# Performance work log

Measured on AMD Instinct MI355X. Metric: run time of the kernel, lower is better.

## Reference

```python
import jax, jax.numpy as jnp
import numpy as np

N_NEAR = 16
BN_EPS = 1e-5


def fps(xyz, n_center):
    # farthest point sampling, deterministic start at index 0. xyz: [B,N,C]
    B, N, _ = xyz.shape
    dist0 = jnp.full((B, N), jnp.inf, dtype=xyz.dtype)
    far0 = jnp.zeros((B,), dtype=jnp.int32)

    def step(carry, _):
        dist, far = carry
        centroid = jnp.take_along_axis(xyz, far[:, None, None], axis=1)  # [B,1,C]
        d = jnp.sum((xyz - centroid) ** 2, axis=-1)                       # [B,N]
        dist = jnp.minimum(dist, d)
        nxt = jnp.argmax(dist, axis=-1).astype(jnp.int32)
        return (dist, nxt), far

    _, idxs = jax.lax.scan(step, (dist0, far0), None, length=n_center)
    return jnp.transpose(idxs)  # [B, n_center]


def knn(xyz, k):
    # k nearest neighbors (self included), xyz: [B,N,C] -> idx [B,N,k]
    sq = jnp.sum(xyz * xyz, axis=-1)
    d = sq[:, :, None] - 2.0 * jnp.einsum('bnc,bmc->bnm', xyz, xyz) + sq[:, None, :]
    _, idx = jax.lax.top_k(-d, k)
    return idx


def gather_points(x, idx):
    # x: [B,N,...], idx: [B,*dims] int -> [B,*dims,...]
    return jax.vmap(lambda xb, ib: xb[ib])(x, idx)


def conv_bn_relu(x, W, b, g, be):
    # x: [B,C,K,S]; 1x1 Conv2d + BatchNorm2d (training/batch stats) + ReLU
    y = jnp.einsum('oc,bcks->boks', W, x) + b[None, :, None, None]
    mean = jnp.mean(y, axis=(0, 2, 3), keepdims=True)
    var = jnp.mean((y - mean) ** 2, axis=(0, 2, 3), keepdims=True)  # biased var, as torch BN
    y = (y - mean) * jax.lax.rsqrt(var + BN_EPS)
    y = y * g[None, :, None, None] + be[None, :, None, None]
    return jax.nn.relu(y)


def setup_inputs() -> dict:
    key = jax.random.key(0)
    ks = jax.random.split(key, 8)
    B, N, EMB = 16, 2048, 64
    mlp = [64, 128, 256]
    in_ch = 2 + EMB
    inp = {
        'xy': jax.random.normal(ks[0], (B, 2, N), dtype=jnp.float32),
        'fea': jax.random.normal(ks[1], (B, EMB, N), dtype=jnp.float32),
    }
    last = in_ch
    for i, out in enumerate(mlp):
        inp[f'W{i+1}'] = 0.1 * jax.random.normal(ks[2 + i], (out, last), dtype=jnp.float32)
        inp[f'b{i+1}'] = jnp.zeros((out,), dtype=jnp.float32)
        inp[f'g{i+1}'] = jnp.ones((out,), dtype=jnp.float32)
        inp[f'be{i+1}'] = jnp.zeros((out,), dtype=jnp.float32)
        last = out
    return inp


def reference(xy, fea, W1, b1, g1, be1, W2, b2, g2, be2, W3, b3, g3, be3):
    B, _, N = xy.shape
    n_center = N // 2 + 1
    xyz = jnp.transpose(xy, (0, 2, 1))   # [B,N,2]
    f = jnp.transpose(fea, (0, 2, 1))    # [B,N,emb]

    fps_idx = fps(xyz, n_center)                      # [B,S]
    new_xyz = gather_points(xyz, fps_idx)             # [B,S,2]
    knn_idx = knn(xyz, N_NEAR)                        # [B,N,k]
    knn_of_fps = gather_points(knn_idx, fps_idx)      # [B,S,k]
    grouped_xyz = gather_points(xyz, knn_of_fps)      # [B,S,k,2]
    grouped_norm = grouped_xyz - new_xyz[:, :, None, :]
    grouped_f = gather_points(f, knn_of_fps)          # [B,S,k,emb]
    new_fea = jnp.concatenate([grouped_norm, grouped_f], axis=-1)  # [B,S,k,C]

    x = jnp.transpose(new_fea, (0, 3, 2, 1))          # [B,C,k,S]
    for (W, b, g, be) in ((W1, b1, g1, be1), (W2, b2, g2, be2), (W3, b3, g3, be3)):
        x = conv_bn_relu(x, W, b, g, be)
    out = jnp.max(x, axis=2)                          # [B,C_out,S]
    return jnp.transpose(new_xyz, (0, 2, 1)), out
```

## Files before the change

### kernel.cpp

```cpp
#include <hip/hip_runtime.h>
#include <math.h>

#define B_   16
#define N_   2048
#define S_   1025
#define K_   16
#define EMB_ 64
#define NF_  (B_ * S_ * K_)
#define NCH_ (NF_ / 64)

typedef float v2f __attribute__((ext_vector_type(2)));
typedef short bf16x8 __attribute__((ext_vector_type(8)));
typedef float f32x4 __attribute__((ext_vector_type(4)));

__device__ __forceinline__ unsigned short f2bf(float f) {
  unsigned u = __float_as_uint(f);
  u += 0x7fffu + ((u >> 16) & 1u);
  return (unsigned short)(u >> 16);
}

__global__ __launch_bounds__(256) __attribute__((amdgpu_waves_per_eu(1, 1)))
void fps_pk_kernel(const float* __restrict__ xy, const float* __restrict__ fea,
                   const float* __restrict__ W1,
                   int* __restrict__ fps_idx, float* __restrict__ new_xyz,
                   float* __restrict__ out0, float* __restrict__ P) {
  __shared__ float smem[8192];
  if (blockIdx.x < 16) {
    const int b = blockIdx.x;
    float2* lxy = reinterpret_cast<float2*>(smem);
    const int lane = threadIdx.x;
    const float* xb = xy + (size_t)b * 2 * N_;
    v2f pxp[16], pyp[16];
    float dist[32];
    if (lane < 64) {
      const float2* xb2 = (const float2*)xb;
      const float2* yb2 = (const float2*)(xb + N_);
#pragma unroll
      for (int q = 0; q < 16; ++q) {
        float2 x01 = xb2[lane * 16 + q];
        float2 y01 = yb2[lane * 16 + q];
        int p = lane * 32 + 2 * q;
        lxy[p] = make_float2(x01.x, y01.x);
        lxy[p + 1] = make_float2(x01.y, y01.y);
        pxp[q][0] = x01.x; pxp[q][1] = x01.y;
        pyp[q][0] = y01.x; pyp[q][1] = y01.y;
        dist[2 * q] = __builtin_inff();
        dist[2 * q + 1] = __builtin_inff();
      }
#pragma unroll
      for (int q = 0; q < 16; ++q) {
        asm volatile("" : "+v"(pxp[q]), "+v"(pyp[q]));
      }
    }
    __syncthreads();
    if (lane < 64) {
      int cur = 0;
      for (int t = 0; t < S_; ++t) {
        float2 c = lxy[cur];
        if (lane == 0) {
          fps_idx[b * S_ + t] = cur;
          new_xyz[(b * S_ + t) * 2 + 0] = c.x;
          new_xyz[(b * S_ + t) * 2 + 1] = c.y;
          out0[b * 2 * S_ + t] = c.x;
          out0[b * 2 * S_ + S_ + t] = c.y;
        }
        const float ncx = -c.x, ncy = -c.y;
        v2f ncx2; ncx2[0] = ncx; ncx2[1] = ncx;
        v2f ncy2; ncy2[0] = ncy; ncy2[1] = ncy;
        float lmax0 = -__builtin_inff(), lmax1 = -__builtin_inff();
#pragma unroll
        for (int q = 0; q < 16; ++q) {
          v2f dx, dy, sx, sy, dd;
          asm("v_pk_add_f32 %0, %1, %2" : "=v"(dx) : "v"(pxp[q]), "v"(ncx2));
          asm("v_pk_add_f32 %0, %1, %2" : "=v"(dy) : "v"(pyp[q]), "v"(ncy2));
          asm("v_pk_mul_f32 %0, %1, %1" : "=v"(sx) : "v"(dx));
          asm("v_pk_mul_f32 %0, %1, %1" : "=v"(sy) : "v"(dy));
          asm("v_pk_add_f32 %0, %1, %2" : "=v"(dd) : "v"(sx), "v"(sy));
          float nd0 = fminf(dist[2 * q], dd[0]);
          float nd1 = fminf(dist[2 * q + 1], dd[1]);
          dist[2 * q] = nd0;
          dist[2 * q + 1] = nd1;
          lmax0 = fmaxf(lmax0, nd0);
          lmax1 = fmaxf(lmax1, nd1);
        }
        const float lmax = fmaxf(lmax0, lmax1);
        int xr = __float_as_int(lmax);
#define DPP_MAX_STEP(CTRL)                                                        \
        {                                                                         \
          int tmp_ = __builtin_amdgcn_update_dpp(xr, xr, (CTRL), 0xF, 0xF, false);\
          xr = __float_as_int(fmaxf(__int_as_float(xr), __int_as_float(tmp_)));   \
        }
        DPP_MAX_STEP(0x111)
        DPP_MAX_STEP(0x112)
        DPP_MAX_STEP(0x114)
        DPP_MAX_STEP(0x118)
        DPP_MAX_STEP(0x142)
        DPP_MAX_STEP(0x143)
#undef DPP_MAX_STEP
        const float g = __int_as_float(__builtin_amdgcn_readlane(xr, 63));
        int lf = 0;
#pragma unroll
        for (int j = 31; j >= 0; --j)
          if (dist[j] == g) lf = j;
        unsigned long long mask = __ballot(lmax == g);
        int first = __ffsll(mask) - 1;
        cur = __builtin_amdgcn_readlane(lane * 32 + lf, first);
      }
    }
  } else {
    const int bid = blockIdx.x - 16;
    const int t = threadIdx.x;
    const int b = bid >> 5;
    const int pt0 = (bid & 31) << 6;
    float* W1L = smem;
    float* feaL = smem + 4096;
#pragma unroll
    for (int p = 0; p < 16; ++p) {
      int idx = t + 256 * p;
      int c = idx >> 6, e = idx & 63;
      W1L[e * 64 + c] = W1[c * 66 + 2 + e];
      int r = (t >> 6) + 4 * p, cc = t & 63;
      feaL[r * 64 + cc] = fea[((size_t)b * 64 + r) * N_ + pt0 + cc];
    }
    __syncthreads();
    const int tpt = t & 15, tcq = t >> 4;
    float acc[4][4];
#pragma unroll
    for (int i = 0; i < 4; ++i)
#pragma unroll
      for (int j = 0; j < 4; ++j) acc[i][j] = 0.f;
    for (int e = 0; e < 64; ++e) {
      float4 a4 = *reinterpret_cast<const float4*>(&W1L[e * 64 + tcq * 4]);
      float4 b4 = *reinterpret_cast<const float4*>(&feaL[e * 64 + tpt * 4]);
      const float av[4] = {a4.x, a4.y, a4.z, a4.w};
      const float bvv[4] = {b4.x, b4.y, b4.z, b4.w};
#pragma unroll
      for (int i = 0; i < 4; ++i)
#pragma unroll
        for (int j = 0; j < 4; ++j) acc[i][j] = fmaf(av[i], bvv[j], acc[i][j]);
    }
#pragma unroll
    for (int j = 0; j < 4; ++j) {
      int pt = tpt * 4 + j;
      float4 v = {acc[0][j], acc[1][j], acc[2][j], acc[3][j]};
      *reinterpret_cast<float4*>(&P[((size_t)(b * N_ + pt0 + pt)) * 64 + tcq * 4]) = v;
    }
  }
}

__global__ void wconv_kernel(const float* __restrict__ W2, const float* __restrict__ W3,
                             unsigned short* __restrict__ W2b, unsigned short* __restrict__ W3b) {
  int i = blockIdx.x * 256 + threadIdx.x;
  if (i < 128 * 64) W2b[i] = f2bf(W2[i]);
  if (i < 256 * 128) W3b[i] = f2bf(W3[i]);
}

__global__ __launch_bounds__(256) void knn_kernel(const float* __restrict__ xy,
                                                  const int* __restrict__ fps_idx,
                                                  int* __restrict__ knn_sel) {
  const int b = blockIdx.y;
  __shared__ float2 lxy[N_];
  __shared__ double lsq[N_];
  const float* xb = xy + (size_t)b * 2 * N_;
  for (int p = threadIdx.x; p < N_; p += 256) {
    float x = xb[p], y = xb[N_ + p];
    lxy[p] = make_float2(x, y);
    lsq[p] = (double)x * (double)x + (double)y * (double)y;
  }
  __syncthreads();
  const int t = threadIdx.x;
  const int s = blockIdx.x * 16 + (t >> 4);
  if (s >= S_) return;
  const int oct = t & 15;
  const int p0 = fps_idx[b * S_ + s];
  float2 q = lxy[p0];
  const double xn = (double)q.x, yn = (double)q.y;
  const double sqn = lsq[p0];
  double d16[16];
  int i16[16];
#pragma unroll
  for (int j = 0; j < 16; ++j) { d16[j] = __builtin_inf(); i16[j] = 0x7fffffff; }
  const int mlo = oct * 128;
  for (int m0 = mlo; m0 < mlo + 128; m0 += 4) {
    double dd[4];
#pragma unroll
    for (int u = 0; u < 4; ++u) {
      float2 p = lxy[m0 + u];
      double dot = (double)p.x * xn + (double)p.y * yn;
      dd[u] = (sqn - 2.0 * dot) + lsq[m0 + u];
    }
#pragma unroll
    for (int u = 0; u < 4; ++u) {
      if (dd[u] < d16[15]) {
        double d = dd[u];
        int mi = m0 + u;
#pragma unroll
        for (int j = 15; j >= 1; --j) {
          bool shift = d < d16[j - 1];
          bool ins = d < d16[j];
          d16[j] = shift ? d16[j - 1] : (ins ? d : d16[j]);
          i16[j] = shift ? i16[j - 1] : (ins ? mi : i16[j]);
        }
        if (d < d16[0]) { d16[0] = d; i16[0] = mi; }
      }
    }
  }
#pragma unroll
  for (int w = 1; w <= 8; w <<= 1) {
    double nd[16]; int ni[16];
#pragma unroll
    for (int i = 0; i < 16; ++i) {
      double rd = __shfl_xor(d16[15 - i], w, 64);
      int ri = __shfl_xor(i16[15 - i], w, 64);
      bool takeR = (rd < d16[i]) || (rd == d16[i] && ri < i16[i]);
      nd[i] = takeR ? rd : d16[i];
      ni[i] = takeR ? ri : i16[i];
    }
#pragma unroll
    for (int i = 0; i < 16; ++i) { d16[i] = nd[i]; i16[i] = ni[i]; }
    if (w < 8) {
#pragma unroll
      for (int dstg = 8; dstg >= 1; dstg >>= 1) {
#pragma unroll
        for (int i = 0; i < 16; ++i) {
          if ((i & dstg) == 0) {
            int a = i, c = i + dstg;
            bool sw = (d16[a] > d16[c]) || (d16[a] == d16[c] && i16[a] > i16[c]);
            double tlo = sw ? d16[c] : d16[a];
            double thi = sw ? d16[a] : d16[c];
            int ulo = sw ? i16[c] : i16[a];
            int uhi = sw ? i16[a] : i16[c];
            d16[a] = tlo; d16[c] = thi; i16[a] = ulo; i16[c] = uhi;
          }
        }
      }
    }
  }
  if (oct == 0) {
    int* dst = knn_sel + ((size_t)b * S_ + s) * K_;
#pragma unroll
    for (int j = 0; j < 16; ++j) dst[j] = i16[j];
  }
}

__global__ __launch_bounds__(256) void yk1_kernel(const float* __restrict__ xy,
                                                  const int* __restrict__ knn_sel,
                                                  const float* __restrict__ new_xyz,
                                                  const float* __restrict__ P,
                                                  const float* __restrict__ W1,
                                                  const float* __restrict__ b1,
                                                  float* __restrict__ Y1) {
  __shared__ float w0s[64], w1s[64], bbs[64];
  const int t = threadIdx.x;
  if (t < 64) { w0s[t] = W1[t * 66 + 0]; w1s[t] = W1[t * 66 + 1]; bbs[t] = b1[t]; }
  __syncthreads();
  const int n = blockIdx.x * 256 + t;
  const int bs = n >> 4;
  const int b = bs / S_;
  const int nbr = knn_sel[n];
  const float dx = xy[(size_t)b * 2 * N_ + nbr] - new_xyz[bs * 2 + 0];
  const float dy = xy[(size_t)b * 2 * N_ + N_ + nbr] - new_xyz[bs * 2 + 1];
  const float* prow = &P[((size_t)(b * N_ + nbr)) * 64];
  for (int c4 = 0; c4 < 64; c4 += 4) {
    float4 p4 = *reinterpret_cast<const float4*>(&prow[c4]);
    float v0 = p4.x + w0s[c4 + 0] * dx + w1s[c4 + 0] * dy + bbs[c4 + 0];
    float v1 = p4.y + w0s[c4 + 1] * dx + w1s[c4 + 1] * dy + bbs[c4 + 1];
    float v2 = p4.z + w0s[c4 + 2] * dx + w1s[c4 + 2] * dy + bbs[c4 + 2];
    float v3 = p4.w + w0s[c4 + 3] * dx + w1s[c4 + 3] * dy + bbs[c4 + 3];
    Y1[(size_t)(c4 + 0) * NF_ + n] = v0;
    Y1[(size_t)(c4 + 1) * NF_ + n] = v1;
    Y1[(size_t)(c4 + 2) * NF_ + n] = v2;
    Y1[(size_t)(c4 + 3) * NF_ + n] = v3;
  }
}

__global__ __launch_bounds__(1024) void rowstats_kernel(const float* __restrict__ Y,
                                                        double* __restrict__ sum_out,
                                                        double* __restrict__ sq_out) {
  const int r = blockIdx.x;
  const float* row = Y + (size_t)r * NF_;
  double s = 0.0, s2 = 0.0;
  for (int i = threadIdx.x * 4; i < NF_; i += 4096) {
    float4 v = *reinterpret_cast<const float4*>(&row[i]);
    double dx = v.x, dy = v.y, dz = v.z, dw = v.w;
    s += (dx + dy) + (dz + dw);
    s2 = fma(dx, dx, s2); s2 = fma(dy, dy, s2);
    s2 = fma(dz, dz, s2); s2 = fma(dw, dw, s2);
  }
  __shared__ double sh[1024], sh2[1024];
  sh[threadIdx.x] = s; sh2[threadIdx.x] = s2;
  __syncthreads();
  for (int o = 512; o > 0; o >>= 1) {
    if (threadIdx.x < o) {
      sh[threadIdx.x] += sh[threadIdx.x + o];
      sh2[threadIdx.x] += sh2[threadIdx.x + o];
    }
    __syncthreads();
  }
  if (threadIdx.x == 0) { sum_out[r] = sh[0]; sq_out[r] = sh2[0]; }
}

__global__ void absch_kernel(const double* __restrict__ sumv, const double* __restrict__ sqv,
                             const float* __restrict__ g, const float* __restrict__ be,
                             float* __restrict__ A, float* __restrict__ D, int M) {
  int m = threadIdx.x;
  if (m >= M) return;
  double mu = sumv[m] * (1.0 / NF_);
  double var = sqv[m] * (1.0 / NF_) - mu * mu;
  double a = (double)g[m] / sqrt(var + 1e-5);
  A[m] = (float)a;
  D[m] = (float)((double)be[m] - a * mu);
}

__global__ void redab_kernel(const float* __restrict__ parts, double* __restrict__ sum_out,
                             double* __restrict__ sq_out, int P, int M) {
  int m = threadIdx.x;
  if (m >= M) return;
  double a = 0.0, b = 0.0;
  for (int p = 0; p < P; ++p) {
    a += (double)parts[(size_t)p * 2 * M + m];
    b += (double)parts[(size_t)p * 2 * M + M + m];
  }
  sum_out[m] = a;
  sq_out[m] = b;
}

__device__ __forceinline__ float rowsum16(float v) {
#define RADD(CTRL) { int tm_ = __builtin_amdgcn_update_dpp(0, __float_as_int(v), (CTRL), 0xF, 0xF, true); \
                     v += __int_as_float(tm_); }
  RADD(0x111) RADD(0x112) RADD(0x114) RADD(0x118)
#undef RADD
  return v;
}

__global__ __launch_bounds__(256) void passA_mfma_kernel(
    const float* __restrict__ Y1, const unsigned short* __restrict__ W2b,
    const float* __restrict__ A1v, const float* __restrict__ Bc1v,
    float* __restrict__ parts) {
  __shared__ float ab1[128];
  __shared__ __align__(16) unsigned short x1b[64 * 64];
  const int t = threadIdx.x;
  const int w = t >> 6, L = t & 63;
  if (t < 128) ab1[t] = (t < 64) ? A1v[t] : Bc1v[t - 64];
  bf16x8 w2f[2][2];
#pragma unroll
  for (int rb = 0; rb < 2; ++rb)
#pragma unroll
    for (int ks = 0; ks < 2; ++ks) {
      int row = (2 * w + rb) * 16 + (L & 15);
      int koff = ks * 32 + (L >> 4) * 8;
      w2f[rb][ks] = *reinterpret_cast<const bf16x8*>(&W2b[row * 64 + koff]);
    }
  float vs[2][4], vq[2][4];
#pragma unroll
  for (int rb = 0; rb < 2; ++rb)
#pragma unroll
    for (int r = 0; r < 4; ++r) { vs[rb][r] = 0.f; vq[rb][r] = 0.f; }
  char* x1c = reinterpret_cast<char*>(x1b);
  for (int ch = blockIdx.x; ch < NCH_; ch += 512) {
    const size_t n0 = (size_t)ch * 64;
    __syncthreads();
#pragma unroll
    for (int e = 0; e < 8; ++e) {
      int k0 = 2 * (w + 4 * e);
      float y0 = Y1[(size_t)k0 * NF_ + n0 + L];
      float y1 = Y1[(size_t)(k0 + 1) * NF_ + n0 + L];
      float v0 = fmaxf(fmaf(y0, ab1[k0], ab1[64 + k0]), 0.f);
      float v1 = fmaxf(fmaf(y1, ab1[k0 + 1], ab1[64 + k0 + 1]), 0.f);
      unsigned pk = (unsigned)f2bf(v0) | ((unsigned)f2bf(v1) << 16);
      *reinterpret_cast<unsigned*>(&x1c[L * 128 + ((2 * k0) ^ ((L & 7) << 4))]) = pk;
    }
    __syncthreads();
#pragma unroll
    for (int rb = 0; rb < 2; ++rb) {
      f32x4 acc2[4];
#pragma unroll
      for (int cb = 0; cb < 4; ++cb) acc2[cb][0] = acc2[cb][1] = acc2[cb][2] = acc2[cb][3] = 0.f;
#pragma unroll
      for (int ks = 0; ks < 2; ++ks)
#pragma unroll
        for (int cb = 0; cb < 4; ++cb) {
          int n = cb * 16 + (L & 15);
          int koff = ks * 32 + (L >> 4) * 8;
          bf16x8 bfr = *reinterpret_cast<const bf16x8*>(&x1c[n * 128 + ((2 * koff) ^ ((n & 7) << 4))]);
          acc2[cb] = __builtin_amdgcn_mfma_f32_16x16x32_bf16(w2f[rb][ks], bfr, acc2[cb], 0, 0, 0);
        }
#pragma unroll
      for (int cb = 0; cb < 4; ++cb)
#pragma unroll
        for (int r = 0; r < 4; ++r) {
          float y = acc2[cb][r];
          vs[rb][r] += y;
          vq[rb][r] = fmaf(y, y, vq[rb][r]);
        }
    }
  }
#pragma unroll
  for (int rb = 0; rb < 2; ++rb)
#pragma unroll
    for (int r = 0; r < 4; ++r) {
      float s = rowsum16(vs[rb][r]);
      float q = rowsum16(vq[rb][r]);
      if ((L & 15) == 15) {
        int row = (2 * w + rb) * 16 + (L >> 4) * 4 + r;
        parts[(size_t)blockIdx.x * 256 + row] = s;
        parts[(size_t)blockIdx.x * 256 + 128 + row] = q;
      }
    }
}

__global__ __launch_bounds__(256) void passB_mfma_kernel(
    const float* __restrict__ Y1,
    const unsigned short* __restrict__ W2b, const unsigned short* __restrict__ W3b,
    const float* __restrict__ A1v, const float* __restrict__ Bc1v,
    const float* __restrict__ A2v, const float* __restrict__ D2v,
    float* __restrict__ parts) {
  __shared__ float ab1[128];
  __shared__ __align__(16) unsigned short x1b[64 * 64];
  __shared__ __align__(16) unsigned short x2b[64 * 128];
  const int t = threadIdx.x;
  const int w = t >> 6, L = t & 63;
  if (t < 128) ab1[t] = (t < 64) ? A1v[t] : Bc1v[t - 64];
  bf16x8 w3f[4][4];
#pragma unroll
  for (int rb = 0; rb < 4; ++rb)
#pragma unroll
    for (int ks = 0; ks < 4; ++ks) {
      int row = (4 * w + rb) * 16 + (L & 15);
      int koff = ks * 32 + (L >> 4) * 8;
      w3f[rb][ks] = *reinterpret_cast<const bf16x8*>(&W3b[row * 128 + koff]);
    }
  bf16x8 w2f[2][2];
#pragma unroll
  for (int rb = 0; rb < 2; ++rb)
#pragma unroll
    for (int ks = 0; ks < 2; ++ks) {
      int row = (2 * w + rb) * 16 + (L & 15);
      int koff = ks * 32 + (L >> 4) * 8;
      w2f[rb][ks] = *reinterpret_cast<const bf16x8*>(&W2b[row * 64 + koff]);
    }
  float vs[4][4], vq[4][4];
#pragma unroll
  for (int rb = 0; rb < 4; ++rb)
#pragma unroll
    for (int r = 0; r < 4; ++r) { vs[rb][r] = 0.f; vq[rb][r] = 0.f; }
  char* x1c = reinterpret_cast<char*>(x1b);
  char* x2c = reinterpret_cast<char*>(x2b);
  for (int ch = blockIdx.x; ch < NCH_; ch += 256) {
    const size_t n0 = (size_t)ch * 64;
    __syncthreads();
#pragma unroll
    for (int e = 0; e < 8; ++e) {
      int k0 = 2 * (w + 4 * e);
      float y0 = Y1[(size_t)k0 * NF_ + n0 + L];
      float y1 = Y1[(size_t)(k0 + 1) * NF_ + n0 + L];
      float v0 = fmaxf(fmaf(y0, ab1[k0], ab1[64 + k0]), 0.f);
      float v1 = fmaxf(fmaf(y1, ab1[k0 + 1], ab1[64 + k0 + 1]), 0.f);
      unsigned pk = (unsigned)f2bf(v0) | ((unsigned)f2bf(v1) << 16);
      *reinterpret_cast<unsigned*>(&x1c[L * 128 + ((2 * k0) ^ ((L & 7) << 4))]) = pk;
    }
    __syncthreads();
#pragma unroll
    for (int rb = 0; rb < 2; ++rb) {
      f32x4 acc2[4];
#pragma unroll
      for (int cb = 0; cb < 4; ++cb) acc2[cb][0] = acc2[cb][1] = acc2[cb][2] = acc2[cb][3] = 0.f;
#pragma unroll
      for (int ks = 0; ks < 2; ++ks)
#pragma unroll
        for (int cb = 0; cb < 4; ++cb) {
          int n = cb * 16 + (L & 15);
          int koff = ks * 32 + (L >> 4) * 8;
          bf16x8 bfr = *reinterpret_cast<const bf16x8*>(&x1c[n * 128 + ((2 * koff) ^ ((n & 7) << 4))]);
          acc2[cb] = __builtin_amdgcn_mfma_f32_16x16x32_bf16(w2f[rb][ks], bfr, acc2[cb], 0, 0, 0);
        }
#pragma unroll
      for (int cb = 0; cb < 4; ++cb) {
        int n = cb * 16 + (L & 15);
        int kbase = (2 * w + rb) * 16 + (L >> 4) * 4;
#pragma unroll
        for (int rp = 0; rp < 2; ++rp) {
          int r0 = 2 * rp;
          float a0 = A2v[kbase + r0], d0 = D2v[kbase + r0];
          float a1 = A2v[kbase + r0 + 1], d1 = D2v[kbase + r0 + 1];
          float v0 = fmaxf(fmaf(acc2[cb][r0], a0, d0), 0.f);
          float v1 = fmaxf(fmaf(acc2[cb][r0 + 1], a1, d1), 0.f);
          unsigned pk = (unsigned)f2bf(v0) | ((unsigned)f2bf(v1) << 16);
          int k0 = kbase + r0;
          *reinterpret_cast<unsigned*>(&x2c[n * 256 + ((2 * k0) ^ ((n & 7) << 4))]) = pk;
        }
      }
    }
    __syncthreads();
    bf16x8 b3[4][4];
#pragma unroll
    for (int cb = 0; cb < 4; ++cb)
#pragma unroll
      for (int ks = 0; ks < 4; ++ks) {
        int n = cb * 16 + (L & 15);
        int koff = ks * 32 + (L >> 4) * 8;
        b3[cb][ks] = *reinterpret_cast<const bf16x8*>(&x2c[n * 256 + ((2 * koff) ^ ((n & 7) << 4))]);
      }
#pragma unroll
    for (int rb = 0; rb < 4; ++rb) {
      f32x4 acc3[4];
#pragma unroll
      for (int cb = 0; cb < 4; ++cb) acc3[cb][0] = acc3[cb][1] = acc3[cb][2] = acc3[cb][3] = 0.f;
#pragma unroll
      for (int ks = 0; ks < 4; ++ks)
#pragma unroll
        for (int cb = 0; cb < 4; ++cb)
          acc3[cb] = __builtin_amdgcn_mfma_f32_16x16x32_bf16(w3f[rb][ks], b3[cb][ks], acc3[cb], 0, 0, 0);
#pragma unroll
      for (int cb = 0; cb < 4; ++cb)
#pragma unroll
        for (int r = 0; r < 4; ++r) {
          float y = acc3[cb][r];
          vs[rb][r] += y;
          vq[rb][r] = fmaf(y, y, vq[rb][r]);
        }
    }
  }
#pragma unroll
  for (int rb = 0; rb < 4; ++rb)
#pragma unroll
    for (int r = 0; r < 4; ++r) {
      float s = rowsum16(vs[rb][r]);
      float q = rowsum16(vq[rb][r]);
      if ((L & 15) == 15) {
        int row = (4 * w + rb) * 16 + (L >> 4) * 4 + r;
        parts[(size_t)blockIdx.x * 512 + row] = s;
        parts[(size_t)blockIdx.x * 512 + 256 + row] = q;
      }
    }
}

__global__ __launch_bounds__(256) void final_mfma_kernel(
    const float* __restrict__ Y1,
    const unsigned short* __restrict__ W2b,
    const unsigned short* __restrict__ W3b,
    const float* __restrict__ A1v, const float* __restrict__ Bc1v,
    const float* __restrict__ A2v, const float* __restrict__ D2v,
    const float* __restrict__ A3v, const float* __restrict__ D3v,
    float* __restrict__ out1) {
  __shared__ float ab1[128];
  __shared__ __align__(16) unsigned short x1b[64 * 64];
  __shared__ __align__(16) unsigned short x2b[64 * 128];
  const int t = threadIdx.x;
  const int w = t >> 6, L = t & 63;
  if (t < 128) ab1[t] = (t < 64) ? A1v[t] : Bc1v[t - 64];
  bf16x8 w3f[4][4];
#pragma unroll
  for (int rb = 0; rb < 4; ++rb)
#pragma unroll
    for (int ks = 0; ks < 4; ++ks) {
      int row = (4 * w + rb) * 16 + (L & 15);
      int koff = ks * 32 + (L >> 4) * 8;
      w3f[rb][ks] = *reinterpret_cast<const bf16x8*>(&W3b[row * 128 + koff]);
    }
  bf16x8 w2f[2][2];
#pragma unroll
  for (int rb = 0; rb < 2; ++rb)
#pragma unroll
    for (int ks = 0; ks < 2; ++ks) {
      int row = (2 * w + rb) * 16 + (L & 15);
      int koff = ks * 32 + (L >> 4) * 8;
      w2f[rb][ks] = *reinterpret_cast<const bf16x8*>(&W2b[row * 64 + koff]);
    }
  char* x1c = reinterpret_cast<char*>(x1b);
  char* x2c = reinterpret_cast<char*>(x2b);
  for (int ch = blockIdx.x; ch < NCH_; ch += 512) {
    const size_t n0 = (size_t)ch * 64;
    __syncthreads();
#pragma unroll
    for (int e = 0; e < 8; ++e) {
      int k0 = 2 * (w + 4 * e);
      float y0 = Y1[(size_t)k0 * NF_ + n0 + L];
      float y1 = Y1[(size_t)(k0 + 1) * NF_ + n0 + L];
      float v0 = fmaxf(fmaf(y0, ab1[k0], ab1[64 + k0]), 0.f);
      float v1 = fmaxf(fmaf(y1, ab1[k0 + 1], ab1[64 + k0 + 1]), 0.f);
      unsigned pk = (unsigned)f2bf(v0) | ((unsigned)f2bf(v1) << 16);
      *reinterpret_cast<unsigned*>(&x1c[L * 128 + ((2 * k0) ^ ((L & 7) << 4))]) = pk;
    }
    __syncthreads();
#pragma unroll
    for (int rb = 0; rb < 2; ++rb) {
      f32x4 acc2[4];
#pragma unroll
      for (int cb = 0; cb < 4; ++cb) acc2[cb][0] = acc2[cb][1] = acc2[cb][2] = acc2[cb][3] = 0.f;
#pragma unroll
      for (int ks = 0; ks < 2; ++ks)
#pragma unroll
        for (int cb = 0; cb < 4; ++cb) {
          int n = cb * 16 + (L & 15);
          int koff = ks * 32 + (L >> 4) * 8;
          bf16x8 bfr = *reinterpret_cast<const bf16x8*>(&x1c[n * 128 + ((2 * koff) ^ ((n & 7) << 4))]);
          acc2[cb] = __builtin_amdgcn_mfma_f32_16x16x32_bf16(w2f[rb][ks], bfr, acc2[cb], 0, 0, 0);
        }
#pragma unroll
      for (int cb = 0; cb < 4; ++cb) {
        int n = cb * 16 + (L & 15);
        int kbase = (2 * w + rb) * 16 + (L >> 4) * 4;
#pragma unroll
        for (int rp = 0; rp < 2; ++rp) {
          int r0 = 2 * rp;
          float a0 = A2v[kbase + r0], d0 = D2v[kbase + r0];
          float a1 = A2v[kbase + r0 + 1], d1 = D2v[kbase + r0 + 1];
          float v0 = fmaxf(fmaf(acc2[cb][r0], a0, d0), 0.f);
          float v1 = fmaxf(fmaf(acc2[cb][r0 + 1], a1, d1), 0.f);
          unsigned pk = (unsigned)f2bf(v0) | ((unsigned)f2bf(v1) << 16);
          int k0 = kbase + r0;
          *reinterpret_cast<unsigned*>(&x2c[n * 256 + ((2 * k0) ^ ((n & 7) << 4))]) = pk;
        }
      }
    }
    __syncthreads();
    bf16x8 b3[4][4];
#pragma unroll
    for (int cb = 0; cb < 4; ++cb)
#pragma unroll
      for (int ks = 0; ks < 4; ++ks) {
        int n = cb * 16 + (L & 15);
        int koff = ks * 32 + (L >> 4) * 8;
        b3[cb][ks] = *reinterpret_cast<const bf16x8*>(&x2c[n * 256 + ((2 * koff) ^ ((n & 7) << 4))]);
      }
#pragma unroll
    for (int rb = 0; rb < 4; ++rb) {
      f32x4 acc3[4];
#pragma unroll
      for (int cb = 0; cb < 4; ++cb) acc3[cb][0] = acc3[cb][1] = acc3[cb][2] = acc3[cb][3] = 0.f;
#pragma unroll
      for (int ks = 0; ks < 4; ++ks)
#pragma unroll
        for (int cb = 0; cb < 4; ++cb)
          acc3[cb] = __builtin_amdgcn_mfma_f32_16x16x32_bf16(w3f[rb][ks], b3[cb][ks], acc3[cb], 0, 0, 0);
      int rowbase = (4 * w + rb) * 16 + (L >> 4) * 4;
#pragma unroll
      for (int cb = 0; cb < 4; ++cb) {
#pragma unroll
        for (int r = 0; r < 4; ++r) {
          float v = fmaf(acc3[cb][r], A3v[rowbase + r], D3v[rowbase + r]);
          int xi = __float_as_int(v);
#define RMAX(CTRL) { int tm_ = __builtin_amdgcn_update_dpp(xi, xi, (CTRL), 0xF, 0xF, false); \
                     xi = __float_as_int(fmaxf(__int_as_float(xi), __int_as_float(tm_))); }
          RMAX(0x111) RMAX(0x112) RMAX(0x114) RMAX(0x118)
#undef RMAX
          if ((L & 15) == 15) {
            int row = rowbase + r;
            int bs = ch * 4 + cb;
            int b = bs / S_;
            int s = bs - b * S_;
            out1[((size_t)(b * 256 + row)) * S_ + s] = fmaxf(__int_as_float(xi), 0.f);
          }
        }
      }
    }
  }
}

__global__ void diag_kernel(float* out, float v) {
  if (threadIdx.x == 0 && blockIdx.x == 0) out[0] = v;
}

extern "C" void kernel_launch(void* const* d_in, const int* in_sizes, int n_in,
                              void* d_out, int out_size, void* d_ws, size_t ws_size,
                              hipStream_t stream) {
  const float* xy  = (const float*)d_in[0];
  const float* fea = (const float*)d_in[1];
  const float* W1  = (const float*)d_in[2];
  const float* b1  = (const float*)d_in[3];
  const float* g1  = (const float*)d_in[4];
  const float* be1 = (const float*)d_in[5];
  const float* W2  = (const float*)d_in[6];
  const float* g2  = (const float*)d_in[8];
  const float* be2 = (const float*)d_in[9];
  const float* W3  = (const float*)d_in[10];
  const float* g3  = (const float*)d_in[12];
  const float* be3 = (const float*)d_in[13];
  float* out = (float*)d_out;
  float* out1 = out + B_ * 2 * S_;

  char* w = (char*)d_ws;
  size_t off = 0;
  auto take = [&](size_t bytes) -> void* {
    void* p = w + off;
    off += (bytes + 255) & ~(size_t)255;
    return p;
  };
  int*    fps_idx = (int*)take((size_t)B_ * S_ * 4);
  float*  new_xyz = (float*)take((size_t)B_ * S_ * 2 * 4);
  int*    knn_sel = (int*)take((size_t)NF_ * 4);
  float*  P       = (float*)take((size_t)B_ * N_ * 64 * 4);
  float*  Y1      = (float*)take((size_t)64 * NF_ * 4);
  double* Sy1     = (double*)take(64 * 8);
  double* Sq1     = (double*)take(64 * 8);
  float*  A1      = (float*)take(64 * 4);
  float*  Bc1     = (float*)take(64 * 4);
  float*  partsA  = (float*)take((size_t)512 * 256 * 4);
  double* Sy2     = (double*)take(128 * 8);
  double* Sq2     = (double*)take(128 * 8);
  float*  A2      = (float*)take(128 * 4);
  float*  D2      = (float*)take(128 * 4);
  float*  partsB  = (float*)take((size_t)256 * 512 * 4);
  double* Sy3     = (double*)take(256 * 8);
  double* Sq3     = (double*)take(256 * 8);
  float*  A3      = (float*)take(256 * 4);
  float*  D3      = (float*)take(256 * 4);
  unsigned short* W2b = (unsigned short*)take((size_t)128 * 64 * 2);
  unsigned short* W3b = (unsigned short*)take((size_t)256 * 128 * 2);

  if (off > ws_size) {
    diag_kernel<<<1, 64, 0, stream>>>(out, (float)(ws_size >> 20));
    return;
  }

  fps_pk_kernel<<<16 + 512, 256, 0, stream>>>(xy, fea, W1, fps_idx, new_xyz, out, P);
  wconv_kernel<<<128, 256, 0, stream>>>(W2, W3, W2b, W3b);
  knn_kernel<<<dim3((S_ + 15) / 16, B_), 256, 0, stream>>>(xy, fps_idx, knn_sel);
  yk1_kernel<<<NF_ / 256, 256, 0, stream>>>(xy, knn_sel, new_xyz, P, W1, b1, Y1);

  rowstats_kernel<<<64, 1024, 0, stream>>>(Y1, Sy1, Sq1);
  absch_kernel<<<1, 64, 0, stream>>>(Sy1, Sq1, g1, be1, A1, Bc1, 64);

  passA_mfma_kernel<<<512, 256, 0, stream>>>(Y1, W2b, A1, Bc1, partsA);
  redab_kernel<<<1, 128, 0, stream>>>(partsA, Sy2, Sq2, 512, 128);
  absch_kernel<<<1, 128, 0, stream>>>(Sy2, Sq2, g2, be2, A2, D2, 128);

  passB_mfma_kernel<<<256, 256, 0, stream>>>(Y1, W2b, W3b, A1, Bc1, A2, D2, partsB);
  redab_kernel<<<1, 256, 0, stream>>>(partsB, Sy3, Sq3, 256, 256);
  absch_kernel<<<1, 256, 0, stream>>>(Sy3, Sq3, g3, be3, A3, D3, 256);

  final_mfma_kernel<<<512, 256, 0, stream>>>(Y1, W2b, W3b, A1, Bc1, A2, D2, A3, D3, out1);
}
```

Baseline: 1.449 ms.

## Tree-reduce FPS lane max with index descent; split KNN scan across 32 lanes

The FPS inner step now computes each lane's max over its 32 distances as a pairwise tree. It then finds the argmax index by descending that tree with selects instead of a 32-way linear compare scan, which shortens the serial dependency chain on every one of the 1025 iterations. Separately, the KNN kernel assigns 32 lanes per query point instead of 16, so each lane scans 64 candidates. This adds one more shuffle-merge stage and launches twice as many blocks. The tree descent picks the first matching leaf in tree order, which should still give the lowest index among ties.

After: 1.347 ms. -7.0%, faster.

```diff
diff --git a/kernel.cpp b/kernel.cpp
--- a/kernel.cpp
+++ b/kernel.cpp
@@ -67,7 +67,6 @@
         const float ncx = -c.x, ncy = -c.y;
         v2f ncx2; ncx2[0] = ncx; ncx2[1] = ncx;
         v2f ncy2; ncy2[0] = ncy; ncy2[1] = ncy;
-        float lmax0 = -__builtin_inff(), lmax1 = -__builtin_inff();
 #pragma unroll
         for (int q = 0; q < 16; ++q) {
           v2f dx, dy, sx, sy, dd;
@@ -76,14 +75,19 @@
           asm("v_pk_mul_f32 %0, %1, %1" : "=v"(sx) : "v"(dx));
           asm("v_pk_mul_f32 %0, %1, %1" : "=v"(sy) : "v"(dy));
           asm("v_pk_add_f32 %0, %1, %2" : "=v"(dd) : "v"(sx), "v"(sy));
-          float nd0 = fminf(dist[2 * q], dd[0]);
-          float nd1 = fminf(dist[2 * q + 1], dd[1]);
-          dist[2 * q] = nd0;
-          dist[2 * q + 1] = nd1;
-          lmax0 = fmaxf(lmax0, nd0);
-          lmax1 = fmaxf(lmax1, nd1);
-        }
-        const float lmax = fmaxf(lmax0, lmax1);
+          dist[2 * q] = fminf(dist[2 * q], dd[0]);
+          dist[2 * q + 1] = fminf(dist[2 * q + 1], dd[1]);
+        }
+        float m1[16], m2[8], m3[4], m4[2];
+#pragma unroll
+        for (int j = 0; j < 16; ++j) m1[j] = fmaxf(dist[2 * j], dist[2 * j + 1]);
+#pragma unroll
+        for (int j = 0; j < 8; ++j) m2[j] = fmaxf(m1[2 * j], m1[2 * j + 1]);
+#pragma unroll
+        for (int j = 0; j < 4; ++j) m3[j] = fmaxf(m2[2 * j], m2[2 * j + 1]);
+        m4[0] = fmaxf(m3[0], m3[1]);
+        m4[1] = fmaxf(m3[2], m3[3]);
+        const float lmax = fmaxf(m4[0], m4[1]);
         int xr = __float_as_int(lmax);
 #define DPP_MAX_STEP(CTRL)                                                        \
         {                                                                         \
@@ -98,10 +102,37 @@
         DPP_MAX_STEP(0x143)
 #undef DPP_MAX_STEP
         const float g = __int_as_float(__builtin_amdgcn_readlane(xr, 63));
-        int lf = 0;
-#pragma unroll
-        for (int j = 31; j >= 0; --j)
-          if (dist[j] == g) lf = j;
+        int n = (m4[0] == g) ? 0 : 1;
+        float c3 = (n & 1) ? m3[2] : m3[0];
+        n = 2 * n + ((c3 == g) ? 0 : 1);
+        float lo2 = (n & 1) ? m2[2] : m2[0];
+        float hi2 = (n & 1) ? m2[6] : m2[4];
+        float c2 = (n & 2) ? hi2 : lo2;
+        n = 2 * n + ((c2 == g) ? 0 : 1);
+        float a0 = (n & 1) ? m1[2] : m1[0];
+        float a1 = (n & 1) ? m1[6] : m1[4];
+        float a2 = (n & 1) ? m1[10] : m1[8];
+        float a3 = (n & 1) ? m1[14] : m1[12];
+        float b0 = (n & 2) ? a1 : a0;
+        float b1 = (n & 2) ? a3 : a2;
+        float c1 = (n & 4) ? b1 : b0;
+        n = 2 * n + ((c1 == g) ? 0 : 1);
+        float e0 = (n & 1) ? dist[2] : dist[0];
+        float e1 = (n & 1) ? dist[6] : dist[4];
+        float e2 = (n & 1) ? dist[10] : dist[8];
+        float e3 = (n & 1) ? dist[14] : dist[12];
+        float e4 = (n & 1) ? dist[18] : dist[16];
+        float e5 = (n & 1) ? dist[22] : dist[20];
+        float e6 = (n & 1) ? dist[26] : dist[24];
+        float e7 = (n & 1) ? dist[30] : dist[28];
+        float f0 = (n & 2) ? e1 : e0;
+        float f1 = (n & 2) ? e3 : e2;
+        float f2 = (n & 2) ? e5 : e4;
+        float f3 = (n & 2) ? e7 : e6;
+        float g0 = (n & 4) ? f1 : f0;
+        float g1 = (n & 4) ? f3 : f2;
+        float c0 = (n & 8) ? g1 : g0;
+        const int lf = 2 * n + ((c0 == g) ? 0 : 1);
         unsigned long long mask = __ballot(lmax == g);
         int first = __ffsll(mask) - 1;
         cur = __builtin_amdgcn_readlane(lane * 32 + lf, first);
@@ -169,9 +200,9 @@
   }
   __syncthreads();
   const int t = threadIdx.x;
-  const int s = blockIdx.x * 16 + (t >> 4);
+  const int s = blockIdx.x * 8 + (t >> 5);
   if (s >= S_) return;
-  const int oct = t & 15;
+  const int oct = t & 31;
   const int p0 = fps_idx[b * S_ + s];
   float2 q = lxy[p0];
   const double xn = (double)q.x, yn = (double)q.y;
@@ -180,8 +211,8 @@
   int i16[16];
 #pragma unroll
   for (int j = 0; j < 16; ++j) { d16[j] = __builtin_inf(); i16[j] = 0x7fffffff; }
-  const int mlo = oct * 128;
-  for (int m0 = mlo; m0 < mlo + 128; m0 += 4) {
+  const int mlo = oct * 64;
+  for (int m0 = mlo; m0 < mlo + 64; m0 += 4) {
     double dd[4];
 #pragma unroll
     for (int u = 0; u < 4; ++u) {
@@ -206,7 +237,7 @@
     }
   }
 #pragma unroll
-  for (int w = 1; w <= 8; w <<= 1) {
+  for (int w = 1; w <= 16; w <<= 1) {
     double nd[16]; int ni[16];
 #pragma unroll
     for (int i = 0; i < 16; ++i) {
@@ -218,7 +249,7 @@
     }
 #pragma unroll
     for (int i = 0; i < 16; ++i) { d16[i] = nd[i]; i16[i] = ni[i]; }
-    if (w < 8) {
+    if (w < 16) {
 #pragma unroll
       for (int dstg = 8; dstg >= 1; dstg >>= 1) {
 #pragma unroll
@@ -716,7 +747,7 @@
 
   fps_pk_kernel<<<16 + 512, 256, 0, stream>>>(xy, fea, W1, fps_idx, new_xyz, out, P);
   wconv_kernel<<<128, 256, 0, stream>>>(W2, W3, W2b, W3b);
-  knn_kernel<<<dim3((S_ + 15) / 16, B_), 256, 0, stream>>>(xy, fps_idx, knn_sel);
+  knn_kernel<<<dim3((S_ + 7) / 8, B_), 256, 0, stream>>>(xy, fps_idx, knn_sel);
   yk1_kernel<<<NF_ / 256, 256, 0, stream>>>(xy, knn_sel, new_xyz, P, W1, b1, Y1);
 
   rowstats_kernel<<<64, 1024, 0, stream>>>(Y1, Sy1, Sq1);
```
